# Kernel tuning notes

Hardware: AMD Instinct MI355X
Metric: run time of the kernel (lower is better)

## Reference

```python
import jax, jax.numpy as jnp
import numpy as np

OUT_SIZE = 224  # hardcoded in the torch forward: F.interpolate(size=224)


def _lin_interp_axis(x, axis, out_size):
    """1D linear interpolation along `axis` with align_corners=True."""
    in_size = x.shape[axis]
    # align_corners=True: src = dst * (in-1)/(out-1)
    pos = jnp.arange(out_size, dtype=jnp.float32) * ((in_size - 1) / (out_size - 1))
    i0 = jnp.clip(jnp.floor(pos).astype(jnp.int32), 0, in_size - 2)
    w = pos - i0.astype(jnp.float32)
    x0 = jnp.take(x, i0, axis=axis)
    x1 = jnp.take(x, i0 + 1, axis=axis)
    bshape = [1] * x.ndim
    bshape[axis] = out_size
    w = w.reshape(bshape)
    return x0 * (1.0 - w) + x1 * w


def setup_inputs() -> dict:
    key = jax.random.key(0)
    k1, k2, k3 = jax.random.split(key, 3)
    hidden, n_classes = 32, 4
    x = jax.random.normal(k1, (1, hidden, 14, 14, 14), dtype=jnp.float32)
    # 1x1x1 conv3d == per-voxel channel matmul; store kernel as [out, in]
    W = jax.random.normal(k2, (n_classes, hidden), dtype=jnp.float32) / np.sqrt(hidden)
    b = jax.random.normal(k3, (n_classes,), dtype=jnp.float32) * 0.01
    return {"x": x, "W": W, "b": b}


def reference(x, W, b):
    # Trilinear upsample (separable linear interp per spatial axis),
    # upsampling smallest dims first keeps peak memory low.
    y = _lin_interp_axis(x, 2, OUT_SIZE)   # [B,C,224,14,14]
    y = _lin_interp_axis(y, 3, OUT_SIZE)   # [B,C,224,224,14]
    y = _lin_interp_axis(y, 4, OUT_SIZE)   # [B,C,224,224,224]
    # 1x1x1 conv3d: per-voxel channel contraction
    z = jnp.einsum('bcdhw,oc->bodhw', y, W) + b[None, :, None, None, None]
    # softmax over channel dim (dim=1)
    return jax.nn.softmax(z, axis=1)
```

## Files before the change

### kernel.cpp

```cpp
#include <hip/hip_runtime.h>
#include <hip/hip_bf16.h>


#define NSP 2744
#define NV  11239424
#define RATIO (13.0f / 223.0f)

__global__ __launch_bounds__(256) void conv_small(
    const float* __restrict__ x,
    const float* __restrict__ W,
    const float* __restrict__ b,
    float4* __restrict__ z)
{
    int s = blockIdx.x * 256 + threadIdx.x;
    if (s >= NSP) return;
    float a0 = b[0], a1 = b[1], a2 = b[2], a3 = b[3];
#pragma unroll
    for (int c = 0; c < 32; ++c) {
        float xv = x[c * NSP + s];
        a0 = fmaf(W[c],      xv, a0);
        a1 = fmaf(W[32 + c], xv, a1);
        a2 = fmaf(W[64 + c], xv, a2);
        a3 = fmaf(W[96 + c], xv, a3);
    }
    z[s] = make_float4(a0, a1, a2, a3);
}

__device__ __forceinline__ float4 bilerp4(const float4* __restrict__ zs,
                                          int b00, int b01, int b10, int b11,
                                          int iw,
                                          float c00, float c01, float c10, float c11)
{
    float4 A = zs[b00 + iw], B = zs[b01 + iw], C = zs[b10 + iw], D = zs[b11 + iw];
    float4 r;
    r.x = fmaf(c11, D.x, fmaf(c10, C.x, fmaf(c01, B.x, c00 * A.x)));
    r.y = fmaf(c11, D.y, fmaf(c10, C.y, fmaf(c01, B.y, c00 * A.y)));
    r.z = fmaf(c11, D.z, fmaf(c10, C.z, fmaf(c01, B.z, c00 * A.z)));
    r.w = fmaf(c11, D.w, fmaf(c10, C.w, fmaf(c01, B.w, c00 * A.w)));
    return r;
}

__global__ __launch_bounds__(512) void upsample_softmax(
    const float4* __restrict__ z,
    float* __restrict__ out)
{
    __shared__ float4 zs[NSP];
    for (int k = threadIdx.x; k < NSP; k += 512) zs[k] = z[k];
    __syncthreads();

    unsigned gid = blockIdx.x * 512u + threadIdx.x;
    unsigned w4  = gid % 56u;
    unsigned row = gid / 56u;
    unsigned hh  = row % 224u;
    unsigned dd  = row / 224u;

    float posd = (float)dd * RATIO;
    int   i0d  = min((int)posd, 12);
    float wd   = posd - (float)i0d;
    float posh = (float)hh * RATIO;
    int   i0h  = min((int)posh, 12);
    float wh   = posh - (float)i0h;

    int   wb    = (int)w4 * 4;
    float posw0 = (float)wb * RATIO;
    int   iw0   = min((int)posw0, 12);

    float c11 = wd * wh;
    float c10 = wd - c11;
    float c01 = wh - c11;
    float c00 = 1.0f - wd - wh + c11;

    int b00 = (i0d * 14 + i0h) * 14;
    int b01 = b00 + 14;
    int b10 = b00 + 196;
    int b11 = b00 + 210;

    float4 g0 = bilerp4(zs, b00, b01, b10, b11, iw0,              c00, c01, c10, c11);
    float4 g1 = bilerp4(zs, b00, b01, b10, b11, iw0 + 1,          c00, c01, c10, c11);
    float4 g2 = bilerp4(zs, b00, b01, b10, b11, min(iw0 + 2, 13), c00, c01, c10, c11);

    float4 d10, d21;
    d10.x = g1.x - g0.x; d10.y = g1.y - g0.y; d10.z = g1.z - g0.z; d10.w = g1.w - g0.w;
    d21.x = g2.x - g1.x; d21.y = g2.y - g1.y; d21.z = g2.z - g1.z; d21.w = g2.w - g1.w;

    const float LOG2E = 1.44269504088896340736f;
    float4 res[4];
#pragma unroll
    for (int j = 0; j < 4; ++j) {
        float posw = (float)(wb + j) * RATIO;
        int   i0w  = min((int)posw, 12);
        float ww   = posw - (float)i0w;
        bool  hi   = (i0w > iw0);
        float bx = hi ? g1.x : g0.x, by = hi ? g1.y : g0.y,
              bz = hi ? g1.z : g0.z, bw = hi ? g1.w : g0.w;
        float ex = hi ? d21.x : d10.x, ey = hi ? d21.y : d10.y,
              ez = hi ? d21.z : d10.z, ew = hi ? d21.w : d10.w;
        float v0 = fmaf(ww, ex, bx);
        float v1 = fmaf(ww, ey, by);
        float v2 = fmaf(ww, ez, bz);
        float v3 = fmaf(ww, ew, bw);
        float t0 = v0 * LOG2E, t1 = v1 * LOG2E, t2 = v2 * LOG2E, t3 = v3 * LOG2E;
        float m  = fmaxf(fmaxf(t0, t1), fmaxf(t2, t3));
        float e0 = exp2f(t0 - m), e1 = exp2f(t1 - m), e2 = exp2f(t2 - m), e3 = exp2f(t3 - m);
        float s  = (e0 + e1) + (e2 + e3);
        float inv = __builtin_amdgcn_rcpf(s);
        res[j].x = e0 * inv;
        res[j].y = e1 * inv;
        res[j].z = e2 * inv;
        res[j].w = e3 * inv;
    }

    unsigned sidx = row * 224u + (unsigned)wb;
    float4 o0 = make_float4(res[0].x, res[1].x, res[2].x, res[3].x);
    float4 o1 = make_float4(res[0].y, res[1].y, res[2].y, res[3].y);
    float4 o2 = make_float4(res[0].z, res[1].z, res[2].z, res[3].z);
    float4 o3 = make_float4(res[0].w, res[1].w, res[2].w, res[3].w);
    *(float4*)(out + 0u * NV + sidx) = o0;
    *(float4*)(out + 1u * NV + sidx) = o1;
    *(float4*)(out + 2u * NV + sidx) = o2;
    *(float4*)(out + 3u * NV + sidx) = o3;
}

extern "C" void kernel_launch(void* const* d_in, const int* in_sizes, int n_in,
                              void* d_out, int out_size, void* d_ws, size_t ws_size,
                              hipStream_t stream) {
    const float* x = (const float*)d_in[0];
    const float* W = (const float*)d_in[1];
    const float* b = (const float*)d_in[2];
    float* out = (float*)d_out;
    float4* z = (float4*)d_ws;

    conv_small<<<(NSP + 255) / 256, 256, 0, stream>>>(x, W, b, z);
    upsample_softmax<<<(NV / 4) / 512, 512, 0, stream>>>(z, out);
}
```

Measured before the change: 182.5 us.

## Fuse conv and upsample-softmax into one per-depth-plane kernel with staged lerp tables

Merges the two launches into one kernel that uses one block per output depth slice. Each block recomputes the channel contraction for the two source planes it needs, interpolates along depth into a shared table, then builds an H-interpolated table of 224x14 entries. The output loop therefore needs only three shared-memory loads per four outputs. The aim is to remove a launch and the global workspace round trip and to cut redundant bilinear work. The cost is a grid of only 224 blocks of 1024 threads, which may underfill the GPU, plus redundant conv work across blocks and extra barriers.

```diff
diff --git a/kernel.cpp b/kernel.cpp
--- a/kernel.cpp
+++ b/kernel.cpp
@@ -1,124 +1,123 @@
 #include <hip/hip_runtime.h>
-#include <hip/hip_bf16.h>
 
 
 #define NSP 2744
-#define NV  11239424
+#define NPLANE 196
+#define NV  11239424u
+#define PLANE_OUT 50176u
 #define RATIO (13.0f / 223.0f)
+#define LOG2E 1.44269504088896340736f
 
-__global__ __launch_bounds__(256) void conv_small(
+__global__ __launch_bounds__(1024) void fused_decoder(
     const float* __restrict__ x,
     const float* __restrict__ W,
     const float* __restrict__ b,
-    float4* __restrict__ z)
-{
-    int s = blockIdx.x * 256 + threadIdx.x;
-    if (s >= NSP) return;
-    float a0 = b[0], a1 = b[1], a2 = b[2], a3 = b[3];
-#pragma unroll
-    for (int c = 0; c < 32; ++c) {
-        float xv = x[c * NSP + s];
-        a0 = fmaf(W[c],      xv, a0);
-        a1 = fmaf(W[32 + c], xv, a1);
-        a2 = fmaf(W[64 + c], xv, a2);
-        a3 = fmaf(W[96 + c], xv, a3);
-    }
-    z[s] = make_float4(a0, a1, a2, a3);
-}
-
-__device__ __forceinline__ float4 bilerp4(const float4* __restrict__ zs,
-                                          int b00, int b01, int b10, int b11,
-                                          int iw,
-                                          float c00, float c01, float c10, float c11)
-{
-    float4 A = zs[b00 + iw], B = zs[b01 + iw], C = zs[b10 + iw], D = zs[b11 + iw];
-    float4 r;
-    r.x = fmaf(c11, D.x, fmaf(c10, C.x, fmaf(c01, B.x, c00 * A.x)));
-    r.y = fmaf(c11, D.y, fmaf(c10, C.y, fmaf(c01, B.y, c00 * A.y)));
-    r.z = fmaf(c11, D.z, fmaf(c10, C.z, fmaf(c01, B.z, c00 * A.z)));
-    r.w = fmaf(c11, D.w, fmaf(c10, C.w, fmaf(c01, B.w, c00 * A.w)));
-    return r;
-}
-
-__global__ __launch_bounds__(512) void upsample_softmax(
-    const float4* __restrict__ z,
     float* __restrict__ out)
 {
-    __shared__ float4 zs[NSP];
-    for (int k = threadIdx.x; k < NSP; k += 512) zs[k] = z[k];
+    __shared__ float4 zloc[2 * NPLANE];
+    __shared__ float4 etab[NPLANE];
+    __shared__ float4 gtab[224 * 15];
+
+    const int   t    = threadIdx.x;
+    const unsigned dd = blockIdx.x;
+    const float posd = (float)dd * RATIO;
+    const int   i0d  = min((int)posd, 12);
+    const float wd   = posd - (float)i0d;
+
+    if (t < 2 * NPLANE) {
+        int pl   = t / NPLANE;
+        int s    = t - pl * NPLANE;
+        int base = (i0d + pl) * NPLANE + s;
+        float a0 = b[0], a1 = b[1], a2 = b[2], a3 = b[3];
+#pragma unroll
+        for (int c = 0; c < 32; ++c) {
+            float xv = x[c * NSP + base];
+            a0 = fmaf(W[c],      xv, a0);
+            a1 = fmaf(W[32 + c], xv, a1);
+            a2 = fmaf(W[64 + c], xv, a2);
+            a3 = fmaf(W[96 + c], xv, a3);
+        }
+        zloc[t] = make_float4(a0, a1, a2, a3);
+    }
     __syncthreads();
 
-    unsigned gid = blockIdx.x * 512u + threadIdx.x;
-    unsigned w4  = gid % 56u;
-    unsigned row = gid / 56u;
-    unsigned hh  = row % 224u;
-    unsigned dd  = row / 224u;
+    if (t < NPLANE) {
+        float4 z0 = zloc[t], z1 = zloc[NPLANE + t];
+        float4 ev;
+        ev.x = fmaf(wd, z1.x - z0.x, z0.x) * LOG2E;
+        ev.y = fmaf(wd, z1.y - z0.y, z0.y) * LOG2E;
+        ev.z = fmaf(wd, z1.z - z0.z, z0.z) * LOG2E;
+        ev.w = fmaf(wd, z1.w - z0.w, z0.w) * LOG2E;
+        etab[t] = ev;
+    }
+    __syncthreads();
 
-    float posd = (float)dd * RATIO;
-    int   i0d  = min((int)posd, 12);
-    float wd   = posd - (float)i0d;
-    float posh = (float)hh * RATIO;
-    int   i0h  = min((int)posh, 12);
-    float wh   = posh - (float)i0h;
+    for (int k = t; k < 224 * 14; k += 1024) {
+        int h  = k / 14;
+        int iw = k - h * 14;
+        float posh = (float)h * RATIO;
+        int   i0h  = min((int)posh, 12);
+        float wh   = posh - (float)i0h;
+        float4 e0 = etab[i0h * 14 + iw];
+        float4 e1 = etab[i0h * 14 + 14 + iw];
+        float4 gv;
+        gv.x = fmaf(wh, e1.x - e0.x, e0.x);
+        gv.y = fmaf(wh, e1.y - e0.y, e0.y);
+        gv.z = fmaf(wh, e1.z - e0.z, e0.z);
+        gv.w = fmaf(wh, e1.w - e0.w, e0.w);
+        gtab[h * 15 + iw] = gv;
+    }
+    __syncthreads();
 
-    int   wb    = (int)w4 * 4;
-    float posw0 = (float)wb * RATIO;
-    int   iw0   = min((int)posw0, 12);
+    const unsigned planeBase = dd * PLANE_OUT;
+    for (int g4 = t; g4 < 12544; g4 += 1024) {
+        int w4 = g4 % 56;
+        int h  = g4 / 56;
+        int wb = w4 * 4;
+        float posw0 = (float)wb * RATIO;
+        int   iw0   = min((int)posw0, 12);
+        float u     = posw0 - (float)iw0;
+        int   gb    = h * 15 + iw0;
+        int   iw2   = min(iw0 + 2, 13);
+        float4 g0 = gtab[gb];
+        float4 g1 = gtab[gb + 1];
+        float4 g2 = gtab[h * 15 + iw2];
 
-    float c11 = wd * wh;
-    float c10 = wd - c11;
-    float c01 = wh - c11;
-    float c00 = 1.0f - wd - wh + c11;
+        float4 d10, d21;
+        d10.x = g1.x - g0.x; d10.y = g1.y - g0.y; d10.z = g1.z - g0.z; d10.w = g1.w - g0.w;
+        d21.x = g2.x - g1.x; d21.y = g2.y - g1.y; d21.z = g2.z - g1.z; d21.w = g2.w - g1.w;
 
-    int b00 = (i0d * 14 + i0h) * 14;
-    int b01 = b00 + 14;
-    int b10 = b00 + 196;
-    int b11 = b00 + 210;
+        float4 res[4];
+#pragma unroll
+        for (int j = 0; j < 4; ++j) {
+            float a  = fminf(u, 1.0f);
+            float bb = u - a;
+            float t0 = fmaf(bb, d21.x, fmaf(a, d10.x, g0.x));
+            float t1 = fmaf(bb, d21.y, fmaf(a, d10.y, g0.y));
+            float t2 = fmaf(bb, d21.z, fmaf(a, d10.z, g0.z));
+            float t3 = fmaf(bb, d21.w, fmaf(a, d10.w, g0.w));
+            float m  = fmaxf(fmaxf(t0, t1), fmaxf(t2, t3));
+            float e0 = exp2f(t0 - m), e1 = exp2f(t1 - m);
+            float e2 = exp2f(t2 - m), e3 = exp2f(t3 - m);
+            float s  = (e0 + e1) + (e2 + e3);
+            float inv = __builtin_amdgcn_rcpf(s);
+            res[j].x = e0 * inv;
+            res[j].y = e1 * inv;
+            res[j].z = e2 * inv;
+            res[j].w = e3 * inv;
+            u += RATIO;
+        }
 
-    float4 g0 = bilerp4(zs, b00, b01, b10, b11, iw0,              c00, c01, c10, c11);
-    float4 g1 = bilerp4(zs, b00, b01, b10, b11, iw0 + 1,          c00, c01, c10, c11);
-    float4 g2 = bilerp4(zs, b00, b01, b10, b11, min(iw0 + 2, 13), c00, c01, c10, c11);
-
-    float4 d10, d21;
-    d10.x = g1.x - g0.x; d10.y = g1.y - g0.y; d10.z = g1.z - g0.z; d10.w = g1.w - g0.w;
-    d21.x = g2.x - g1.x; d21.y = g2.y - g1.y; d21.z = g2.z - g1.z; d21.w = g2.w - g1.w;
-
-    const float LOG2E = 1.44269504088896340736f;
-    float4 res[4];
-#pragma unroll
-    for (int j = 0; j < 4; ++j) {
-        float posw = (float)(wb + j) * RATIO;
-        int   i0w  = min((int)posw, 12);
-        float ww   = posw - (float)i0w;
-        bool  hi   = (i0w > iw0);
-        float bx = hi ? g1.x : g0.x, by = hi ? g1.y : g0.y,
-              bz = hi ? g1.z : g0.z, bw = hi ? g1.w : g0.w;
-        float ex = hi ? d21.x : d10.x, ey = hi ? d21.y : d10.y,
-              ez = hi ? d21.z : d10.z, ew = hi ? d21.w : d10.w;
-        float v0 = fmaf(ww, ex, bx);
-        float v1 = fmaf(ww, ey, by);
-        float v2 = fmaf(ww, ez, bz);
-        float v3 = fmaf(ww, ew, bw);
-        float t0 = v0 * LOG2E, t1 = v1 * LOG2E, t2 = v2 * LOG2E, t3 = v3 * LOG2E;
-        float m  = fmaxf(fmaxf(t0, t1), fmaxf(t2, t3));
-        float e0 = exp2f(t0 - m), e1 = exp2f(t1 - m), e2 = exp2f(t2 - m), e3 = exp2f(t3 - m);
-        float s  = (e0 + e1) + (e2 + e3);
-        float inv = __builtin_amdgcn_rcpf(s);
-        res[j].x = e0 * inv;
-        res[j].y = e1 * inv;
-        res[j].z = e2 * inv;
-        res[j].w = e3 * inv;
+        unsigned sidx = planeBase + (unsigned)h * 224u + (unsigned)wb;
+        float4 o0 = make_float4(res[0].x, res[1].x, res[2].x, res[3].x);
+        float4 o1 = make_float4(res[0].y, res[1].y, res[2].y, res[3].y);
+        float4 o2 = make_float4(res[0].z, res[1].z, res[2].z, res[3].z);
+        float4 o3 = make_float4(res[0].w, res[1].w, res[2].w, res[3].w);
+        *(float4*)(out + 0u * NV + sidx) = o0;
+        *(float4*)(out + 1u * NV + sidx) = o1;
+        *(float4*)(out + 2u * NV + sidx) = o2;
+        *(float4*)(out + 3u * NV + sidx) = o3;
     }
-
-    unsigned sidx = row * 224u + (unsigned)wb;
-    float4 o0 = make_float4(res[0].x, res[1].x, res[2].x, res[3].x);
-    float4 o1 = make_float4(res[0].y, res[1].y, res[2].y, res[3].y);
-    float4 o2 = make_float4(res[0].z, res[1].z, res[2].z, res[3].z);
-    float4 o3 = make_float4(res[0].w, res[1].w, res[2].w, res[3].w);
-    *(float4*)(out + 0u * NV + sidx) = o0;
-    *(float4*)(out + 1u * NV + sidx) = o1;
-    *(float4*)(out + 2u * NV + sidx) = o2;
-    *(float4*)(out + 3u * NV + sidx) = o3;
 }
 
 extern "C" void kernel_launch(void* const* d_in, const int* in_sizes, int n_in,
@@ -128,8 +127,7 @@
     const float* W = (const float*)d_in[1];
     const float* b = (const float*)d_in[2];
     float* out = (float*)d_out;
-    float4* z = (float4*)d_ws;
+    (void)d_ws; (void)ws_size;
 
-    conv_small<<<(NSP + 255) / 256, 256, 0, stream>>>(x, W, b, z);
-    upsample_softmax<<<(NV / 4) / 512, 512, 0, stream>>>(z, out);
+    fused_decoder<<<224, 1024, 0, stream>>>(x, W, b, out);
 }
```

Result: no change. 183.4 us (+0.5%).

## Restructure upsample-softmax so each thread writes contiguous 8-float chunks per class

Applied to the files above, without the earlier changes.

The upsample+softmax kernel now assigns each thread 8 consecutive outputs of a single class plane, so each thread writes 32 contiguous bytes instead of scattering four float4 stores across class planes. The shared-memory staging of the conv result is dropped in favour of direct cached global loads. LOG2E is folded into the conv output and the softmax max-subtraction is removed. The trade-off is that each thread recomputes all four class exponentials to get one class value, quadrupling interpolation and exp work, and skipping the max makes exp overflow possible for large logits.

```diff
diff --git a/kernel.cpp b/kernel.cpp
--- a/kernel.cpp
+++ b/kernel.cpp
@@ -1,10 +1,12 @@
 #include <hip/hip_runtime.h>
-#include <hip/hip_bf16.h>
 
 
 #define NSP 2744
-#define NV  11239424
+#define NPLANE 196
+#define NV 11239424u
+#define GPC 1404928u
 #define RATIO (13.0f / 223.0f)
+#define LOG2E 1.44269504088896340736f
 
 __global__ __launch_bounds__(256) void conv_small(
     const float* __restrict__ x,
@@ -23,15 +25,15 @@
         a2 = fmaf(W[64 + c], xv, a2);
         a3 = fmaf(W[96 + c], xv, a3);
     }
-    z[s] = make_float4(a0, a1, a2, a3);
+    z[s] = make_float4(a0 * LOG2E, a1 * LOG2E, a2 * LOG2E, a3 * LOG2E);
 }
 
 __device__ __forceinline__ float4 bilerp4(const float4* __restrict__ zs,
-                                          int b00, int b01, int b10, int b11,
-                                          int iw,
+                                          int b00, int iw,
                                           float c00, float c01, float c10, float c11)
 {
-    float4 A = zs[b00 + iw], B = zs[b01 + iw], C = zs[b10 + iw], D = zs[b11 + iw];
+    float4 A = zs[b00 + iw], B = zs[b00 + 14 + iw];
+    float4 C = zs[b00 + 196 + iw], D = zs[b00 + 210 + iw];
     float4 r;
     r.x = fmaf(c11, D.x, fmaf(c10, C.x, fmaf(c01, B.x, c00 * A.x)));
     r.y = fmaf(c11, D.y, fmaf(c10, C.y, fmaf(c01, B.y, c00 * A.y)));
@@ -40,17 +42,15 @@
     return r;
 }
 
-__global__ __launch_bounds__(512) void upsample_softmax(
+__global__ __launch_bounds__(256) void store_stream(
     const float4* __restrict__ z,
     float* __restrict__ out)
 {
-    __shared__ float4 zs[NSP];
-    for (int k = threadIdx.x; k < NSP; k += 512) zs[k] = z[k];
-    __syncthreads();
-
-    unsigned gid = blockIdx.x * 512u + threadIdx.x;
-    unsigned w4  = gid % 56u;
-    unsigned row = gid / 56u;
+    unsigned gid = blockIdx.x * 256u + threadIdx.x;
+    unsigned c   = gid / GPC;
+    unsigned rem = gid - c * GPC;
+    unsigned row = rem / 28u;
+    unsigned w8  = (rem - row * 28u) * 8u;
     unsigned hh  = row % 224u;
     unsigned dd  = row / 224u;
 
@@ -61,64 +61,44 @@
     int   i0h  = min((int)posh, 12);
     float wh   = posh - (float)i0h;
 
-    int   wb    = (int)w4 * 4;
-    float posw0 = (float)wb * RATIO;
-    int   iw0   = min((int)posw0, 12);
-
     float c11 = wd * wh;
     float c10 = wd - c11;
     float c01 = wh - c11;
     float c00 = 1.0f - wd - wh + c11;
 
+    float posw0 = (float)w8 * RATIO;
+    int   iw0   = min((int)posw0, 12);
+    float u     = posw0 - (float)iw0;
+
     int b00 = (i0d * 14 + i0h) * 14;
-    int b01 = b00 + 14;
-    int b10 = b00 + 196;
-    int b11 = b00 + 210;
-
-    float4 g0 = bilerp4(zs, b00, b01, b10, b11, iw0,              c00, c01, c10, c11);
-    float4 g1 = bilerp4(zs, b00, b01, b10, b11, iw0 + 1,          c00, c01, c10, c11);
-    float4 g2 = bilerp4(zs, b00, b01, b10, b11, min(iw0 + 2, 13), c00, c01, c10, c11);
+    float4 g0 = bilerp4(z, b00, iw0,              c00, c01, c10, c11);
+    float4 g1 = bilerp4(z, b00, iw0 + 1,          c00, c01, c10, c11);
+    float4 g2 = bilerp4(z, b00, min(iw0 + 2, 13), c00, c01, c10, c11);
 
     float4 d10, d21;
     d10.x = g1.x - g0.x; d10.y = g1.y - g0.y; d10.z = g1.z - g0.z; d10.w = g1.w - g0.w;
     d21.x = g2.x - g1.x; d21.y = g2.y - g1.y; d21.z = g2.z - g1.z; d21.w = g2.w - g1.w;
 
-    const float LOG2E = 1.44269504088896340736f;
-    float4 res[4];
+    float r[8];
 #pragma unroll
-    for (int j = 0; j < 4; ++j) {
-        float posw = (float)(wb + j) * RATIO;
-        int   i0w  = min((int)posw, 12);
-        float ww   = posw - (float)i0w;
-        bool  hi   = (i0w > iw0);
-        float bx = hi ? g1.x : g0.x, by = hi ? g1.y : g0.y,
-              bz = hi ? g1.z : g0.z, bw = hi ? g1.w : g0.w;
-        float ex = hi ? d21.x : d10.x, ey = hi ? d21.y : d10.y,
-              ez = hi ? d21.z : d10.z, ew = hi ? d21.w : d10.w;
-        float v0 = fmaf(ww, ex, bx);
-        float v1 = fmaf(ww, ey, by);
-        float v2 = fmaf(ww, ez, bz);
-        float v3 = fmaf(ww, ew, bw);
-        float t0 = v0 * LOG2E, t1 = v1 * LOG2E, t2 = v2 * LOG2E, t3 = v3 * LOG2E;
-        float m  = fmaxf(fmaxf(t0, t1), fmaxf(t2, t3));
-        float e0 = exp2f(t0 - m), e1 = exp2f(t1 - m), e2 = exp2f(t2 - m), e3 = exp2f(t3 - m);
+    for (int j = 0; j < 8; ++j) {
+        float a  = fminf(u, 1.0f);
+        float bb = u - a;
+        float t0 = fmaf(bb, d21.x, fmaf(a, d10.x, g0.x));
+        float t1 = fmaf(bb, d21.y, fmaf(a, d10.y, g0.y));
+        float t2 = fmaf(bb, d21.z, fmaf(a, d10.z, g0.z));
+        float t3 = fmaf(bb, d21.w, fmaf(a, d10.w, g0.w));
+        float e0 = exp2f(t0), e1 = exp2f(t1), e2 = exp2f(t2), e3 = exp2f(t3);
         float s  = (e0 + e1) + (e2 + e3);
         float inv = __builtin_amdgcn_rcpf(s);
-        res[j].x = e0 * inv;
-        res[j].y = e1 * inv;
-        res[j].z = e2 * inv;
-        res[j].w = e3 * inv;
+        float ec = (c == 0u) ? e0 : (c == 1u) ? e1 : (c == 2u) ? e2 : e3;
+        r[j] = ec * inv;
+        u += RATIO;
     }
 
-    unsigned sidx = row * 224u + (unsigned)wb;
-    float4 o0 = make_float4(res[0].x, res[1].x, res[2].x, res[3].x);
-    float4 o1 = make_float4(res[0].y, res[1].y, res[2].y, res[3].y);
-    float4 o2 = make_float4(res[0].z, res[1].z, res[2].z, res[3].z);
-    float4 o3 = make_float4(res[0].w, res[1].w, res[2].w, res[3].w);
-    *(float4*)(out + 0u * NV + sidx) = o0;
-    *(float4*)(out + 1u * NV + sidx) = o1;
-    *(float4*)(out + 2u * NV + sidx) = o2;
-    *(float4*)(out + 3u * NV + sidx) = o3;
+    float4* dst = (float4*)(out + (size_t)gid * 8u);
+    dst[0] = make_float4(r[0], r[1], r[2], r[3]);
+    dst[1] = make_float4(r[4], r[5], r[6], r[7]);
 }
 
 extern "C" void kernel_launch(void* const* d_in, const int* in_sizes, int n_in,
@@ -131,5 +111,5 @@
     float4* z = (float4*)d_ws;
 
     conv_small<<<(NSP + 255) / 256, 256, 0, stream>>>(x, W, b, z);
-    upsample_softmax<<<(NV / 4) / 512, 512, 0, stream>>>(z, out);
+    store_stream<<<21952, 256, 0, stream>>>(z, out);
 }
```

After: 218.6 us. 1.2x slower.
